# Performance work log

Hardware: AMD Instinct MI355X
Metric: run time of the kernel (lower is better)

The kernel has to match this reference:

```python
import jax, jax.numpy as jnp
import numpy as np

# cv2 GrabCut label codes
GC_BGD, GC_FGD, GC_PR_BGD, GC_PR_FGD = 0, 1, 2, 3
ITER_COUNT = 5
GAMMA = 50.0  # smoothness weight (GrabCut's standard gamma)

B, C, H, W = 2, 256, 512, 512


def setup_inputs() -> dict:
    key = jax.random.key(0)
    k1, k2 = jax.random.split(key)
    features = jax.random.normal(k1, (B, C, H, W), dtype=jnp.float32)
    mask = jax.random.randint(k2, (B, H, W), 0, 2, dtype=jnp.int32)
    return {"features": features, "mask": mask}


def _neighbor_mean(a):
    # a: (B,H,W); 4-neighbor mean with edge replication (smoothness/pairwise term)
    p = jnp.pad(a, ((0, 0), (1, 1), (1, 1)), mode="edge")
    return (p[:, :-2, 1:-1] + p[:, 2:, 1:-1] + p[:, 1:-1, :-2] + p[:, 1:-1, 2:]) * 0.25


def reference(features, mask):
    b, c, h, w = features.shape
    # take first 3 channels as pseudo-RGB image, HWC layout
    img = jnp.transpose(features[:, :3], (0, 2, 3, 1))  # (B,H,W,3)
    # cv2.normalize(..., 0, 255, NORM_MINMAX) over the whole array, then uint8 cast
    mn = img.min(axis=(1, 2, 3), keepdims=True)
    mx = img.max(axis=(1, 2, 3), keepdims=True)
    img = jnp.clip(jnp.floor((img - mn) / (mx - mn + 1e-12) * 255.0), 0.0, 255.0)

    # trimap seeding exactly as in the torch module
    tri = jnp.where(mask == 1, GC_PR_FGD, GC_PR_BGD).astype(jnp.int32)
    bh, bw = int(h * 0.1), int(w * 0.1)
    tri = tri.at[:, :bh, :].set(GC_BGD)
    tri = tri.at[:, h - bh:, :].set(GC_BGD)
    tri = tri.at[:, :, :bw].set(GC_BGD)
    tri = tri.at[:, :, w - bw:].set(GC_BGD)
    tri = tri.at[:, int(h * 0.45):int(h * 0.55), int(w * 0.45):int(w * 0.55)].set(GC_FGD)

    fixed = (tri == GC_BGD) | (tri == GC_FGD)          # hard constraints never change
    fixed_fg = (tri == GC_FGD).astype(img.dtype)
    alpha = ((tri == GC_FGD) | (tri == GC_PR_FGD)).astype(img.dtype)  # fg indicator

    # GrabCut surrogate: iteratively (1) refit fg/bg color models from current
    # labeling (GMM step collapsed to per-region mean), (2) relabel probable
    # pixels by unary (color distance) + pairwise (neighbor agreement) energy
    # -- an ICM approximation of the min-cut step.
    for _ in range(ITER_COUNT):
        a4 = alpha[..., None]                                    # (B,H,W,1)
        fg_mean = (img * a4).sum((1, 2)) / (a4.sum((1, 2)) + 1e-6)        # (B,3)
        bg_mean = (img * (1.0 - a4)).sum((1, 2)) / ((1.0 - a4).sum((1, 2)) + 1e-6)
        d_fg = ((img - fg_mean[:, None, None, :]) ** 2).sum(-1)  # (B,H,W)
        d_bg = ((img - bg_mean[:, None, None, :]) ** 2).sum(-1)
        nb = _neighbor_mean(alpha)
        score = d_bg - d_fg + GAMMA * (2.0 * nb - 1.0)           # >0 -> foreground
        new_alpha = (score > 0).astype(img.dtype)
        alpha = jnp.where(fixed, fixed_fg, new_alpha)

    return alpha  # (B,H,W) in {0,1}, float32
```

## Files before the change

kernel.cpp:

```cpp
#include <hip/hip_runtime.h>
#include <stdint.h>
#include <stddef.h>

#pragma clang fp contract(off)

#define HH 512
#define WW 512
#define HW_ 262144
#define FEAT_BSTRIDE (256*HW_)

__device__ __forceinline__ float quantf(float f, float mn, float denom) {
  float v = (f - mn) / denom * 255.0f;
  v = floorf(v);
  return fminf(fmaxf(v, 0.0f), 255.0f);
}

__device__ __forceinline__ bool is_center(int y, int x) {
  return (y >= 230) & (y < 281) & (x >= 230) & (x < 281);
}
__device__ __forceinline__ bool is_border(int y, int x) {
  return (y < 51) | (y >= 461) | (x < 51) | (x >= 461);
}

__global__ __launch_bounds__(256) void k_minmax(const float* __restrict__ feat,
                                                float2* __restrict__ mm) {
  int blk = blockIdx.x, tid = threadIdx.x;
  int b = blk >> 7, ib = blk & 127;
  const float4* base =
      reinterpret_cast<const float4*>(feat + (size_t)b * FEAT_BSTRIDE) + (size_t)ib * 1536;
  float mn = 3.4e38f, mx = -3.4e38f;
#pragma unroll
  for (int j = 0; j < 6; j++) {
    float4 v = base[tid + j * 256];
    mn = fminf(mn, fminf(fminf(v.x, v.y), fminf(v.z, v.w)));
    mx = fmaxf(mx, fmaxf(fmaxf(v.x, v.y), fmaxf(v.z, v.w)));
  }
  __shared__ float smn[256], smx[256];
  smn[tid] = mn; smx[tid] = mx;
  __syncthreads();
  for (int s = 128; s >= 1; s >>= 1) {
    if (tid < s) {
      smn[tid] = fminf(smn[tid], smn[tid + s]);
      smx[tid] = fmaxf(smx[tid], smx[tid + s]);
    }
    __syncthreads();
  }
  if (tid == 0) mm[blk] = make_float2(smn[0], smx[0]);
}

__global__ __launch_bounds__(256) void k_init(const float* __restrict__ feat,
                                              const int* __restrict__ mask,
                                              const float2* __restrict__ mm,
                                              uint32_t* __restrict__ packed,
                                              uint8_t* __restrict__ alphaA,
                                              int4* __restrict__ totals,
                                              int4* __restrict__ slot0) {
  int blk = blockIdx.x, tid = threadIdx.x;
  int b = blk >> 7;
  __shared__ float smn[128], smx[128];
  if (tid < 128) { float2 v = mm[b * 128 + tid]; smn[tid] = v.x; smx[tid] = v.y; }
  __syncthreads();
  for (int s = 64; s >= 1; s >>= 1) {
    if (tid < s) {
      smn[tid] = fminf(smn[tid], smn[tid + s]);
      smx[tid] = fmaxf(smx[tid], smx[tid + s]);
    }
    __syncthreads();
  }
  float mn = smn[0];
  float denom = (smx[0] - mn) + 1e-12f;
  const float* fb = feat + (size_t)b * FEAT_BSTRIDE;
  int a0 = 0, a1 = 0, a2 = 0, a3 = 0, t0 = 0, t1 = 0, t2 = 0;
#pragma unroll
  for (int j = 0; j < 8; j++) {
    int p = blk * 2048 + tid + j * 256;
    int pb = p & (HW_ - 1);
    int y = pb >> 9, x = pb & 511;
    int r  = (int)quantf(fb[pb], mn, denom);
    int g  = (int)quantf(fb[HW_ + pb], mn, denom);
    int bl = (int)quantf(fb[2 * HW_ + pb], mn, denom);
    packed[p] = (uint32_t)r | ((uint32_t)g << 8) | ((uint32_t)bl << 16);
    int a;
    if (is_center(y, x)) a = 1;
    else if (is_border(y, x)) a = 0;
    else a = (mask[p] == 1) ? 1 : 0;
    alphaA[p] = (uint8_t)a;
    a0 += r * a; a1 += g * a; a2 += bl * a; a3 += a;
    t0 += r; t1 += g; t2 += bl;
  }
  __shared__ int red[256][8];
  red[tid][0] = a0; red[tid][1] = a1; red[tid][2] = a2; red[tid][3] = a3;
  red[tid][4] = t0; red[tid][5] = t1; red[tid][6] = t2; red[tid][7] = 0;
  __syncthreads();
  for (int s = 128; s >= 1; s >>= 1) {
    if (tid < s) {
#pragma unroll
      for (int j = 0; j < 7; j++) red[tid][j] += red[tid + s][j];
    }
    __syncthreads();
  }
  if (tid == 0) {
    slot0[blk]  = make_int4(red[0][0], red[0][1], red[0][2], red[0][3]);
    totals[blk] = make_int4(red[0][4], red[0][5], red[0][6], 0);
  }
}

__global__ __launch_bounds__(256) void k_relabel(const uint32_t* __restrict__ packed,
                                                 const uint8_t* __restrict__ ain,
                                                 uint8_t* __restrict__ aout,
                                                 const int4* __restrict__ totals,
                                                 const int4* __restrict__ slotIn,
                                                 int4* __restrict__ slotOut,
                                                 float* __restrict__ out,
                                                 int finalIter) {
  int blk = blockIdx.x, tid = threadIdx.x;
  int b = blk >> 7;
  __shared__ int red[128][8];
  if (tid < 128) {
    int4 s = slotIn[b * 128 + tid];
    int4 t = totals[b * 128 + tid];
    red[tid][0] = s.x; red[tid][1] = s.y; red[tid][2] = s.z; red[tid][3] = s.w;
    red[tid][4] = t.x; red[tid][5] = t.y; red[tid][6] = t.z; red[tid][7] = 0;
  }
  __syncthreads();
  for (int s = 64; s >= 1; s >>= 1) {
    if (tid < s) {
#pragma unroll
      for (int j = 0; j < 7; j++) red[tid][j] += red[tid + s][j];
    }
    __syncthreads();
  }
  __shared__ float fmv[3], bmv[3];
  if (tid == 0) {
    int cnt = red[0][3];
    float fden = (float)cnt + 1e-6f;
    float bden = (float)(HW_ - cnt) + 1e-6f;
#pragma unroll
    for (int c = 0; c < 3; c++) {
      fmv[c] = (float)red[0][c] / fden;
      bmv[c] = (float)(red[0][4 + c] - red[0][c]) / bden;
    }
  }
  __syncthreads();
  float f0 = fmv[0], f1 = fmv[1], f2 = fmv[2];
  float g0 = bmv[0], g1 = bmv[1], g2 = bmv[2];
  int a0 = 0, a1 = 0, a2 = 0, a3 = 0;
#pragma unroll
  for (int j = 0; j < 8; j++) {
    int p = blk * 2048 + tid + j * 256;
    int pb = p & (HW_ - 1);
    int y = pb >> 9, x = pb & 511;
    uint32_t rgb = packed[p];
    int ri = (int)(rgb & 255u);
    int gi = (int)((rgb >> 8) & 255u);
    int bi = (int)((rgb >> 16) & 255u);
    float i0 = (float)ri, i1 = (float)gi, i2 = (float)bi;
    int up = ain[p - (y > 0 ? WW : 0)];
    int dn = ain[p + (y < HH - 1 ? WW : 0)];
    int lf = ain[p - (x > 0 ? 1 : 0)];
    int rt = ain[p + (x < WW - 1 ? 1 : 0)];
    float nb = (float)(((up + dn) + lf) + rt) * 0.25f;
    float pair = 50.0f * ((2.0f * nb) - 1.0f);
    float t0 = i0 - f0, t1 = i1 - f1, t2 = i2 - f2;
    float df = ((t0 * t0) + (t1 * t1)) + (t2 * t2);
    float u0 = i0 - g0, u1 = i1 - g1, u2 = i2 - g2;
    float db = ((u0 * u0) + (u1 * u1)) + (u2 * u2);
    float score = (db - df) + pair;
    int a;
    if (is_center(y, x)) a = 1;
    else if (is_border(y, x)) a = 0;
    else a = (score > 0.0f) ? 1 : 0;
    aout[p] = (uint8_t)a;
    if (finalIter) out[p] = (float)a;
    a0 += ri * a; a1 += gi * a; a2 += bi * a; a3 += a;
  }
  __shared__ int red2[256][4];
  red2[tid][0] = a0; red2[tid][1] = a1; red2[tid][2] = a2; red2[tid][3] = a3;
  __syncthreads();
  for (int s = 128; s >= 1; s >>= 1) {
    if (tid < s) {
#pragma unroll
      for (int j = 0; j < 4; j++) red2[tid][j] += red2[tid + s][j];
    }
    __syncthreads();
  }
  if (tid == 0) slotOut[blk] = make_int4(red2[0][0], red2[0][1], red2[0][2], red2[0][3]);
}

extern "C" void kernel_launch(void* const* d_in, const int* in_sizes, int n_in,
                              void* d_out, int out_size, void* d_ws, size_t ws_size,
                              hipStream_t stream) {
  const float* feat = (const float*)d_in[0];
  const int*   mask = (const int*)d_in[1];
  float* out = (float*)d_out;

  char* ws = (char*)d_ws;
  uint8_t*  aA     = (uint8_t*)(ws);
  uint8_t*  aB     = (uint8_t*)(ws + 524288);
  float2*   mm     = (float2*)(ws + 1048576);
  int4*     totals = (int4*)(ws + 1050624);
  int4*     slots  = (int4*)(ws + 1054720);
  uint32_t* packed = (uint32_t*)(ws + 1079296);

  k_minmax<<<256, 256, 0, stream>>>(feat, mm);
  k_init<<<256, 256, 0, stream>>>(feat, mask, mm, packed, aA, totals, slots );

  uint8_t* ain = aA;
  uint8_t* aout_buf = aB;
  for (int k = 0; k < 5; k++) {
    k_relabel<<<256, 256, 0, stream>>>(packed, ain, aout_buf, totals,
                                       slots + (size_t)k * 256,
                                       slots + (size_t)(k + 1) * 256,
                                       out, (k == 4) ? 1 : 0);
    uint8_t* tmp = ain; ain = aout_buf; aout_buf = tmp;
  }
}
```

Baseline: 611.3 us.

## Fuse all stages into one cooperative kernel with grid syncs and register-held pixels

Replaces the seven kernel launches (minmax, init, five relabels) with one cooperative kernel that uses grid-wide syncs between phases. Each thread keeps its RGB values, packed quantized colors and trimap codes in registers, so the packed buffer and the repeated mask and feature reads are gone. The min/max pass now reads only the three channel planes it needs for the assigned pixels, where the old pass read a flat float4 span. The cost is cooperative launch overhead and grid barriers, plus higher register pressure.

```diff
diff --git a/kernel.cpp b/kernel.cpp
--- a/kernel.cpp
+++ b/kernel.cpp
@@ -1,8 +1,11 @@
 #include <hip/hip_runtime.h>
+#include <hip/hip_cooperative_groups.h>
 #include <stdint.h>
 #include <stddef.h>
 
 #pragma clang fp contract(off)
+
+namespace cg = cooperative_groups;
 
 #define HH 512
 #define WW 512
@@ -22,20 +25,40 @@
   return (y < 51) | (y >= 461) | (x < 51) | (x >= 461);
 }
 
-__global__ __launch_bounds__(256) void k_minmax(const float* __restrict__ feat,
-                                                float2* __restrict__ mm) {
-  int blk = blockIdx.x, tid = threadIdx.x;
-  int b = blk >> 7, ib = blk & 127;
-  const float4* base =
-      reinterpret_cast<const float4*>(feat + (size_t)b * FEAT_BSTRIDE) + (size_t)ib * 1536;
+__global__ __launch_bounds__(256) void k_fused(
+    const float* __restrict__ feat, const int* __restrict__ mask,
+    float* __restrict__ out,
+    uint8_t* __restrict__ aA, uint8_t* __restrict__ aB,
+    float2* __restrict__ mm, int4* __restrict__ totals,
+    int4* __restrict__ slots)
+{
+  cg::grid_group grid = cg::this_grid();
+  const int blk = blockIdx.x, tid = threadIdx.x;
+  const int b = blk >> 7;
+  const float* fbp = feat + (size_t)b * FEAT_BSTRIDE;
+
+  __shared__ float smn[256], smx[256];
+  __shared__ int red[256][8];
+  __shared__ float fmv[3], bmv[3];
+
+  float fr[8], fg[8], fbl[8];
+  uint32_t code = 0;
   float mn = 3.4e38f, mx = -3.4e38f;
 #pragma unroll
-  for (int j = 0; j < 6; j++) {
-    float4 v = base[tid + j * 256];
-    mn = fminf(mn, fminf(fminf(v.x, v.y), fminf(v.z, v.w)));
-    mx = fmaxf(mx, fmaxf(fmaxf(v.x, v.y), fmaxf(v.z, v.w)));
-  }
-  __shared__ float smn[256], smx[256];
+  for (int j = 0; j < 8; j++) {
+    int p = blk * 2048 + tid + j * 256;
+    int pb = p & (HW_ - 1);
+    int y = pb >> 9, x = pb & 511;
+    float r = fbp[pb], g = fbp[HW_ + pb], bl = fbp[2 * HW_ + pb];
+    fr[j] = r; fg[j] = g; fbl[j] = bl;
+    mn = fminf(mn, fminf(r, fminf(g, bl)));
+    mx = fmaxf(mx, fmaxf(r, fmaxf(g, bl)));
+    uint32_t c2;
+    if (is_center(y, x)) c2 = 1u;
+    else if (is_border(y, x)) c2 = 2u;
+    else c2 = (mask[p] == 1) ? 3u : 0u;
+    code |= c2 << (2 * j);
+  }
   smn[tid] = mn; smx[tid] = mx;
   __syncthreads();
   for (int s = 128; s >= 1; s >>= 1) {
@@ -46,18 +69,9 @@
     __syncthreads();
   }
   if (tid == 0) mm[blk] = make_float2(smn[0], smx[0]);
-}
-
-__global__ __launch_bounds__(256) void k_init(const float* __restrict__ feat,
-                                              const int* __restrict__ mask,
-                                              const float2* __restrict__ mm,
-                                              uint32_t* __restrict__ packed,
-                                              uint8_t* __restrict__ alphaA,
-                                              int4* __restrict__ totals,
-                                              int4* __restrict__ slot0) {
-  int blk = blockIdx.x, tid = threadIdx.x;
-  int b = blk >> 7;
-  __shared__ float smn[128], smx[128];
+  __threadfence();
+  grid.sync();
+
   if (tid < 128) { float2 v = mm[b * 128 + tid]; smn[tid] = v.x; smx[tid] = v.y; }
   __syncthreads();
   for (int s = 64; s >= 1; s >>= 1) {
@@ -67,30 +81,28 @@
     }
     __syncthreads();
   }
-  float mn = smn[0];
-  float denom = (smx[0] - mn) + 1e-12f;
-  const float* fb = feat + (size_t)b * FEAT_BSTRIDE;
-  int a0 = 0, a1 = 0, a2 = 0, a3 = 0, t0 = 0, t1 = 0, t2 = 0;
-#pragma unroll
-  for (int j = 0; j < 8; j++) {
-    int p = blk * 2048 + tid + j * 256;
-    int pb = p & (HW_ - 1);
-    int y = pb >> 9, x = pb & 511;
-    int r  = (int)quantf(fb[pb], mn, denom);
-    int g  = (int)quantf(fb[HW_ + pb], mn, denom);
-    int bl = (int)quantf(fb[2 * HW_ + pb], mn, denom);
-    packed[p] = (uint32_t)r | ((uint32_t)g << 8) | ((uint32_t)bl << 16);
-    int a;
-    if (is_center(y, x)) a = 1;
-    else if (is_border(y, x)) a = 0;
-    else a = (mask[p] == 1) ? 1 : 0;
-    alphaA[p] = (uint8_t)a;
-    a0 += r * a; a1 += g * a; a2 += bl * a; a3 += a;
-    t0 += r; t1 += g; t2 += bl;
-  }
-  __shared__ int red[256][8];
-  red[tid][0] = a0; red[tid][1] = a1; red[tid][2] = a2; red[tid][3] = a3;
-  red[tid][4] = t0; red[tid][5] = t1; red[tid][6] = t2; red[tid][7] = 0;
+  float bmn = smn[0];
+  float denom = (smx[0] - bmn) + 1e-12f;
+
+  uint32_t pk[8];
+  {
+    int a0 = 0, a1 = 0, a2 = 0, a3 = 0, t0 = 0, t1 = 0, t2 = 0;
+#pragma unroll
+    for (int j = 0; j < 8; j++) {
+      int p = blk * 2048 + tid + j * 256;
+      int r  = (int)quantf(fr[j],  bmn, denom);
+      int g  = (int)quantf(fg[j],  bmn, denom);
+      int bl = (int)quantf(fbl[j], bmn, denom);
+      pk[j] = (uint32_t)r | ((uint32_t)g << 8) | ((uint32_t)bl << 16);
+      uint32_t c2 = (code >> (2 * j)) & 3u;
+      int a = (c2 == 1u || c2 == 3u) ? 1 : 0;
+      aA[p] = (uint8_t)a;
+      a0 += r * a; a1 += g * a; a2 += bl * a; a3 += a;
+      t0 += r; t1 += g; t2 += bl;
+    }
+    red[tid][0] = a0; red[tid][1] = a1; red[tid][2] = a2; red[tid][3] = a3;
+    red[tid][4] = t0; red[tid][5] = t1; red[tid][6] = t2; red[tid][7] = 0;
+  }
   __syncthreads();
   for (int s = 128; s >= 1; s >>= 1) {
     if (tid < s) {
@@ -100,91 +112,88 @@
     __syncthreads();
   }
   if (tid == 0) {
-    slot0[blk]  = make_int4(red[0][0], red[0][1], red[0][2], red[0][3]);
+    slots[blk]  = make_int4(red[0][0], red[0][1], red[0][2], red[0][3]);
     totals[blk] = make_int4(red[0][4], red[0][5], red[0][6], 0);
   }
-}
-
-__global__ __launch_bounds__(256) void k_relabel(const uint32_t* __restrict__ packed,
-                                                 const uint8_t* __restrict__ ain,
-                                                 uint8_t* __restrict__ aout,
-                                                 const int4* __restrict__ totals,
-                                                 const int4* __restrict__ slotIn,
-                                                 int4* __restrict__ slotOut,
-                                                 float* __restrict__ out,
-                                                 int finalIter) {
-  int blk = blockIdx.x, tid = threadIdx.x;
-  int b = blk >> 7;
-  __shared__ int red[128][8];
-  if (tid < 128) {
-    int4 s = slotIn[b * 128 + tid];
-    int4 t = totals[b * 128 + tid];
-    red[tid][0] = s.x; red[tid][1] = s.y; red[tid][2] = s.z; red[tid][3] = s.w;
-    red[tid][4] = t.x; red[tid][5] = t.y; red[tid][6] = t.z; red[tid][7] = 0;
-  }
-  __syncthreads();
-  for (int s = 64; s >= 1; s >>= 1) {
-    if (tid < s) {
-#pragma unroll
-      for (int j = 0; j < 7; j++) red[tid][j] += red[tid + s][j];
-    }
-    __syncthreads();
-  }
-  __shared__ float fmv[3], bmv[3];
-  if (tid == 0) {
-    int cnt = red[0][3];
-    float fden = (float)cnt + 1e-6f;
-    float bden = (float)(HW_ - cnt) + 1e-6f;
-#pragma unroll
-    for (int c = 0; c < 3; c++) {
-      fmv[c] = (float)red[0][c] / fden;
-      bmv[c] = (float)(red[0][4 + c] - red[0][c]) / bden;
-    }
-  }
-  __syncthreads();
-  float f0 = fmv[0], f1 = fmv[1], f2 = fmv[2];
-  float g0 = bmv[0], g1 = bmv[1], g2 = bmv[2];
-  int a0 = 0, a1 = 0, a2 = 0, a3 = 0;
-#pragma unroll
-  for (int j = 0; j < 8; j++) {
-    int p = blk * 2048 + tid + j * 256;
-    int pb = p & (HW_ - 1);
-    int y = pb >> 9, x = pb & 511;
-    uint32_t rgb = packed[p];
-    int ri = (int)(rgb & 255u);
-    int gi = (int)((rgb >> 8) & 255u);
-    int bi = (int)((rgb >> 16) & 255u);
-    float i0 = (float)ri, i1 = (float)gi, i2 = (float)bi;
-    int up = ain[p - (y > 0 ? WW : 0)];
-    int dn = ain[p + (y < HH - 1 ? WW : 0)];
-    int lf = ain[p - (x > 0 ? 1 : 0)];
-    int rt = ain[p + (x < WW - 1 ? 1 : 0)];
-    float nb = (float)(((up + dn) + lf) + rt) * 0.25f;
-    float pair = 50.0f * ((2.0f * nb) - 1.0f);
-    float t0 = i0 - f0, t1 = i1 - f1, t2 = i2 - f2;
-    float df = ((t0 * t0) + (t1 * t1)) + (t2 * t2);
-    float u0 = i0 - g0, u1 = i1 - g1, u2 = i2 - g2;
-    float db = ((u0 * u0) + (u1 * u1)) + (u2 * u2);
-    float score = (db - df) + pair;
-    int a;
-    if (is_center(y, x)) a = 1;
-    else if (is_border(y, x)) a = 0;
-    else a = (score > 0.0f) ? 1 : 0;
-    aout[p] = (uint8_t)a;
-    if (finalIter) out[p] = (float)a;
-    a0 += ri * a; a1 += gi * a; a2 += bi * a; a3 += a;
-  }
-  __shared__ int red2[256][4];
-  red2[tid][0] = a0; red2[tid][1] = a1; red2[tid][2] = a2; red2[tid][3] = a3;
-  __syncthreads();
-  for (int s = 128; s >= 1; s >>= 1) {
-    if (tid < s) {
-#pragma unroll
-      for (int j = 0; j < 4; j++) red2[tid][j] += red2[tid + s][j];
-    }
-    __syncthreads();
-  }
-  if (tid == 0) slotOut[blk] = make_int4(red2[0][0], red2[0][1], red2[0][2], red2[0][3]);
+  __threadfence();
+  grid.sync();
+
+  uint8_t* ain = aA;
+  uint8_t* aout = aB;
+  for (int k = 0; k < 5; k++) {
+    const int4* slotIn = slots + (size_t)k * 256;
+    int4* slotOut = slots + (size_t)(k + 1) * 256;
+    if (tid < 128) {
+      int4 s = slotIn[b * 128 + tid];
+      int4 t = totals[b * 128 + tid];
+      red[tid][0] = s.x; red[tid][1] = s.y; red[tid][2] = s.z; red[tid][3] = s.w;
+      red[tid][4] = t.x; red[tid][5] = t.y; red[tid][6] = t.z; red[tid][7] = 0;
+    }
+    __syncthreads();
+    for (int s = 64; s >= 1; s >>= 1) {
+      if (tid < s) {
+#pragma unroll
+        for (int j = 0; j < 7; j++) red[tid][j] += red[tid + s][j];
+      }
+      __syncthreads();
+    }
+    if (tid == 0) {
+      int cnt = red[0][3];
+      float fden = (float)cnt + 1e-6f;
+      float bden = (float)(HW_ - cnt) + 1e-6f;
+#pragma unroll
+      for (int c = 0; c < 3; c++) {
+        fmv[c] = (float)red[0][c] / fden;
+        bmv[c] = (float)(red[0][4 + c] - red[0][c]) / bden;
+      }
+    }
+    __syncthreads();
+    float f0 = fmv[0], f1 = fmv[1], f2 = fmv[2];
+    float g0 = bmv[0], g1 = bmv[1], g2 = bmv[2];
+    int a0 = 0, a1 = 0, a2 = 0, a3 = 0;
+#pragma unroll
+    for (int j = 0; j < 8; j++) {
+      int p = blk * 2048 + tid + j * 256;
+      int pb = p & (HW_ - 1);
+      int y = pb >> 9, x = pb & 511;
+      uint32_t rgb = pk[j];
+      int ri = (int)(rgb & 255u);
+      int gi = (int)((rgb >> 8) & 255u);
+      int bi = (int)((rgb >> 16) & 255u);
+      float i0 = (float)ri, i1 = (float)gi, i2 = (float)bi;
+      int up = ain[p - (y > 0 ? WW : 0)];
+      int dn = ain[p + (y < HH - 1 ? WW : 0)];
+      int lf = ain[p - (x > 0 ? 1 : 0)];
+      int rt = ain[p + (x < WW - 1 ? 1 : 0)];
+      float nb = (float)(((up + dn) + lf) + rt) * 0.25f;
+      float pair = 50.0f * ((2.0f * nb) - 1.0f);
+      float t0 = i0 - f0, t1 = i1 - f1, t2 = i2 - f2;
+      float df = ((t0 * t0) + (t1 * t1)) + (t2 * t2);
+      float u0 = i0 - g0, u1 = i1 - g1, u2 = i2 - g2;
+      float db = ((u0 * u0) + (u1 * u1)) + (u2 * u2);
+      float score = (db - df) + pair;
+      uint32_t c2 = (code >> (2 * j)) & 3u;
+      int a;
+      if (c2 == 1u) a = 1;
+      else if (c2 == 2u) a = 0;
+      else a = (score > 0.0f) ? 1 : 0;
+      aout[p] = (uint8_t)a;
+      if (k == 4) out[p] = (float)a;
+      a0 += ri * a; a1 += gi * a; a2 += bi * a; a3 += a;
+    }
+    red[tid][0] = a0; red[tid][1] = a1; red[tid][2] = a2; red[tid][3] = a3;
+    __syncthreads();
+    for (int s = 128; s >= 1; s >>= 1) {
+      if (tid < s) {
+#pragma unroll
+        for (int j = 0; j < 4; j++) red[tid][j] += red[tid + s][j];
+      }
+      __syncthreads();
+    }
+    if (tid == 0) slotOut[blk] = make_int4(red[0][0], red[0][1], red[0][2], red[0][3]);
+    if (k < 4) { __threadfence(); grid.sync(); }
+    uint8_t* t = ain; ain = aout; aout = t;
+  }
 }
 
 extern "C" void kernel_launch(void* const* d_in, const int* in_sizes, int n_in,
@@ -195,23 +204,14 @@
   float* out = (float*)d_out;
 
   char* ws = (char*)d_ws;
-  uint8_t*  aA     = (uint8_t*)(ws);
-  uint8_t*  aB     = (uint8_t*)(ws + 524288);
-  float2*   mm     = (float2*)(ws + 1048576);
-  int4*     totals = (int4*)(ws + 1050624);
-  int4*     slots  = (int4*)(ws + 1054720);
-  uint32_t* packed = (uint32_t*)(ws + 1079296);
-
-  k_minmax<<<256, 256, 0, stream>>>(feat, mm);
-  k_init<<<256, 256, 0, stream>>>(feat, mask, mm, packed, aA, totals, slots );
-
-  uint8_t* ain = aA;
-  uint8_t* aout_buf = aB;
-  for (int k = 0; k < 5; k++) {
-    k_relabel<<<256, 256, 0, stream>>>(packed, ain, aout_buf, totals,
-                                       slots + (size_t)k * 256,
-                                       slots + (size_t)(k + 1) * 256,
-                                       out, (k == 4) ? 1 : 0);
-    uint8_t* tmp = ain; ain = aout_buf; aout_buf = tmp;
-  }
-}
+  uint8_t* aA     = (uint8_t*)(ws);
+  uint8_t* aB     = (uint8_t*)(ws + 524288);
+  float2*  mm     = (float2*)(ws + 1048576);
+  int4*    totals = (int4*)(ws + 1050624);
+  int4*    slots  = (int4*)(ws + 1054720);
+
+  void* args[] = {(void*)&feat, (void*)&mask, (void*)&out, (void*)&aA, (void*)&aB,
+                  (void*)&mm, (void*)&totals, (void*)&slots};
+  hipLaunchCooperativeKernel((const void*)k_fused, dim3(256), dim3(256),
+                             args, 0, stream);
+}
```

After: 875.7 us. 1.43x slower.

## Vectorize init/relabel, stage alpha rows in LDS, use wave-shuffle reductions

Applied to the files above, without the earlier changes.

Init and relabel now process four contiguous pixels per thread with float4/uint4/uint32 vector loads and stores, and launch 512 blocks instead of 256. Relabel stages the up, center and down alpha rows for its two output rows into shared memory, so neighbor lookups become packed-byte extracts instead of scattered byte loads. The shared-memory tree reductions are replaced by wavefront shuffle sums plus a small cross-wave combine, which cuts barrier count. The slot and packed workspace offsets are moved to fit the doubled number of per-block partials.

```diff
diff --git a/kernel.cpp b/kernel.cpp
--- a/kernel.cpp
+++ b/kernel.cpp
@@ -20,6 +20,12 @@
 }
 __device__ __forceinline__ bool is_border(int y, int x) {
   return (y < 51) | (y >= 461) | (x < 51) | (x >= 461);
+}
+
+__device__ __forceinline__ int wsum(int v) {
+#pragma unroll
+  for (int m = 32; m >= 1; m >>= 1) v += __shfl_xor(v, m);
+  return v;
 }
 
 __global__ __launch_bounds__(256) void k_minmax(const float* __restrict__ feat,
@@ -56,7 +62,7 @@
                                               int4* __restrict__ totals,
                                               int4* __restrict__ slot0) {
   int blk = blockIdx.x, tid = threadIdx.x;
-  int b = blk >> 7;
+  int b = blk >> 8;
   __shared__ float smn[128], smx[128];
   if (tid < 128) { float2 v = mm[b * 128 + tid]; smn[tid] = v.x; smx[tid] = v.y; }
   __syncthreads();
@@ -69,39 +75,58 @@
   }
   float mn = smn[0];
   float denom = (smx[0] - mn) + 1e-12f;
-  const float* fb = feat + (size_t)b * FEAT_BSTRIDE;
+
+  int pix = blk * 1024 + tid * 4;
+  int pb = pix & (HW_ - 1);
+  int y = pb >> 9, xb = pb & 511;
+  const float* fbp = feat + (size_t)b * FEAT_BSTRIDE;
+  float4 cr = *reinterpret_cast<const float4*>(fbp + pb);
+  float4 cg = *reinterpret_cast<const float4*>(fbp + HW_ + pb);
+  float4 cb = *reinterpret_cast<const float4*>(fbp + 2 * HW_ + pb);
+  int4 mk = *reinterpret_cast<const int4*>(mask + pix);
+  float rs[4] = {cr.x, cr.y, cr.z, cr.w};
+  float gs[4] = {cg.x, cg.y, cg.z, cg.w};
+  float bs[4] = {cb.x, cb.y, cb.z, cb.w};
+  int mks[4] = {mk.x, mk.y, mk.z, mk.w};
   int a0 = 0, a1 = 0, a2 = 0, a3 = 0, t0 = 0, t1 = 0, t2 = 0;
-#pragma unroll
-  for (int j = 0; j < 8; j++) {
-    int p = blk * 2048 + tid + j * 256;
-    int pb = p & (HW_ - 1);
-    int y = pb >> 9, x = pb & 511;
-    int r  = (int)quantf(fb[pb], mn, denom);
-    int g  = (int)quantf(fb[HW_ + pb], mn, denom);
-    int bl = (int)quantf(fb[2 * HW_ + pb], mn, denom);
-    packed[p] = (uint32_t)r | ((uint32_t)g << 8) | ((uint32_t)bl << 16);
+  uint32_t pkw[4];
+  uint32_t aw = 0;
+#pragma unroll
+  for (int i = 0; i < 4; i++) {
+    int r  = (int)quantf(rs[i], mn, denom);
+    int g  = (int)quantf(gs[i], mn, denom);
+    int bl = (int)quantf(bs[i], mn, denom);
+    pkw[i] = (uint32_t)r | ((uint32_t)g << 8) | ((uint32_t)bl << 16);
+    int x = xb + i;
     int a;
     if (is_center(y, x)) a = 1;
     else if (is_border(y, x)) a = 0;
-    else a = (mask[p] == 1) ? 1 : 0;
-    alphaA[p] = (uint8_t)a;
+    else a = (mks[i] == 1) ? 1 : 0;
+    aw |= (uint32_t)a << (8 * i);
     a0 += r * a; a1 += g * a; a2 += bl * a; a3 += a;
     t0 += r; t1 += g; t2 += bl;
   }
-  __shared__ int red[256][8];
-  red[tid][0] = a0; red[tid][1] = a1; red[tid][2] = a2; red[tid][3] = a3;
-  red[tid][4] = t0; red[tid][5] = t1; red[tid][6] = t2; red[tid][7] = 0;
-  __syncthreads();
-  for (int s = 128; s >= 1; s >>= 1) {
-    if (tid < s) {
-#pragma unroll
-      for (int j = 0; j < 7; j++) red[tid][j] += red[tid + s][j];
+  *reinterpret_cast<uint4*>(packed + pix) = make_uint4(pkw[0], pkw[1], pkw[2], pkw[3]);
+  *reinterpret_cast<uint32_t*>(alphaA + pix) = aw;
+
+  a0 = wsum(a0); a1 = wsum(a1); a2 = wsum(a2); a3 = wsum(a3);
+  t0 = wsum(t0); t1 = wsum(t1); t2 = wsum(t2);
+  __shared__ int xw[4][8];
+  int wid = tid >> 6, lane = tid & 63;
+  if (lane == 0) {
+    xw[wid][0] = a0; xw[wid][1] = a1; xw[wid][2] = a2; xw[wid][3] = a3;
+    xw[wid][4] = t0; xw[wid][5] = t1; xw[wid][6] = t2;
+  }
+  __syncthreads();
+  if (tid == 0) {
+    int s0 = 0, s1 = 0, s2 = 0, s3 = 0, u0 = 0, u1 = 0, u2 = 0;
+#pragma unroll
+    for (int w = 0; w < 4; w++) {
+      s0 += xw[w][0]; s1 += xw[w][1]; s2 += xw[w][2]; s3 += xw[w][3];
+      u0 += xw[w][4]; u1 += xw[w][5]; u2 += xw[w][6];
     }
-    __syncthreads();
-  }
-  if (tid == 0) {
-    slot0[blk]  = make_int4(red[0][0], red[0][1], red[0][2], red[0][3]);
-    totals[blk] = make_int4(red[0][4], red[0][5], red[0][6], 0);
+    slot0[blk]  = make_int4(s0, s1, s2, s3);
+    totals[blk] = make_int4(u0, u1, u2, 0);
   }
 }
 
@@ -114,51 +139,74 @@
                                                  float* __restrict__ out,
                                                  int finalIter) {
   int blk = blockIdx.x, tid = threadIdx.x;
-  int b = blk >> 7;
-  __shared__ int red[128][8];
-  if (tid < 128) {
-    int4 s = slotIn[b * 128 + tid];
-    int4 t = totals[b * 128 + tid];
-    red[tid][0] = s.x; red[tid][1] = s.y; red[tid][2] = s.z; red[tid][3] = s.w;
-    red[tid][4] = t.x; red[tid][5] = t.y; red[tid][6] = t.z; red[tid][7] = 0;
-  }
-  __syncthreads();
-  for (int s = 64; s >= 1; s >>= 1) {
-    if (tid < s) {
-#pragma unroll
-      for (int j = 0; j < 7; j++) red[tid][j] += red[tid + s][j];
-    }
-    __syncthreads();
-  }
-  __shared__ float fmv[3], bmv[3];
-  if (tid == 0) {
-    int cnt = red[0][3];
-    float fden = (float)cnt + 1e-6f;
-    float bden = (float)(HW_ - cnt) + 1e-6f;
-#pragma unroll
-    for (int c = 0; c < 3; c++) {
-      fmv[c] = (float)red[0][c] / fden;
-      bmv[c] = (float)(red[0][4 + c] - red[0][c]) / bden;
-    }
-  }
-  __syncthreads();
-  float f0 = fmv[0], f1 = fmv[1], f2 = fmv[2];
-  float g0 = bmv[0], g1 = bmv[1], g2 = bmv[2];
+  int b = blk >> 8;
+  int r0 = (blk & 255) * 2;
+
+  __shared__ uint32_t arowW[4 * 128];
+  {
+    int row_i = tid >> 6;
+    int src_row = r0 - 1 + row_i;
+    src_row = src_row < 0 ? 0 : (src_row > 511 ? 511 : src_row);
+    reinterpret_cast<uint2*>(arowW)[tid] = *reinterpret_cast<const uint2*>(
+        ain + (size_t)b * HW_ + src_row * 512 + (tid & 63) * 8);
+  }
+
+  int4 sv = slotIn[b * 256 + tid];
+  int4 tv = totals[b * 256 + tid];
+  int v0 = wsum(sv.x), v1 = wsum(sv.y), v2 = wsum(sv.z), v3 = wsum(sv.w);
+  int v4 = wsum(tv.x), v5 = wsum(tv.y), v6 = wsum(tv.z);
+  __shared__ int xw[4][8];
+  int wid = tid >> 6, lane = tid & 63;
+  if (lane == 0) {
+    xw[wid][0] = v0; xw[wid][1] = v1; xw[wid][2] = v2; xw[wid][3] = v3;
+    xw[wid][4] = v4; xw[wid][5] = v5; xw[wid][6] = v6;
+  }
+  __syncthreads();
+  int s0 = xw[0][0] + xw[1][0] + xw[2][0] + xw[3][0];
+  int s1 = xw[0][1] + xw[1][1] + xw[2][1] + xw[3][1];
+  int s2 = xw[0][2] + xw[1][2] + xw[2][2] + xw[3][2];
+  int s3 = xw[0][3] + xw[1][3] + xw[2][3] + xw[3][3];
+  int s4 = xw[0][4] + xw[1][4] + xw[2][4] + xw[3][4];
+  int s5 = xw[0][5] + xw[1][5] + xw[2][5] + xw[3][5];
+  int s6 = xw[0][6] + xw[1][6] + xw[2][6] + xw[3][6];
+  int cnt = s3;
+  float fden = (float)cnt + 1e-6f;
+  float bden = (float)(HW_ - cnt) + 1e-6f;
+  float f0 = (float)s0 / fden;
+  float f1 = (float)s1 / fden;
+  float f2 = (float)s2 / fden;
+  float g0 = (float)(s4 - s0) / bden;
+  float g1 = (float)(s5 - s1) / bden;
+  float g2 = (float)(s6 - s2) / bden;
+
+  int lr = tid >> 7;
+  int q  = tid & 127;
+  int x0 = q * 4;
+  int yy = r0 + lr;
+  uint32_t uw = arowW[lr * 128 + q];
+  uint32_t cw = arowW[(lr + 1) * 128 + q];
+  uint32_t dw = arowW[(lr + 2) * 128 + q];
+  const uint8_t* arowB = reinterpret_cast<const uint8_t*>(arowW);
+  int lfb = arowB[(lr + 1) * 512 + (x0 > 0 ? x0 - 1 : 0)];
+  int rtb = arowB[(lr + 1) * 512 + (x0 + 4 < 512 ? x0 + 4 : 511)];
+
+  int pix = b * HW_ + yy * 512 + x0;
+  uint4 pk4 = *reinterpret_cast<const uint4*>(packed + pix);
+  uint32_t pka[4] = {pk4.x, pk4.y, pk4.z, pk4.w};
   int a0 = 0, a1 = 0, a2 = 0, a3 = 0;
-#pragma unroll
-  for (int j = 0; j < 8; j++) {
-    int p = blk * 2048 + tid + j * 256;
-    int pb = p & (HW_ - 1);
-    int y = pb >> 9, x = pb & 511;
-    uint32_t rgb = packed[p];
+  uint32_t awout = 0;
+  float fouts[4];
+#pragma unroll
+  for (int i = 0; i < 4; i++) {
+    uint32_t rgb = pka[i];
     int ri = (int)(rgb & 255u);
     int gi = (int)((rgb >> 8) & 255u);
     int bi = (int)((rgb >> 16) & 255u);
     float i0 = (float)ri, i1 = (float)gi, i2 = (float)bi;
-    int up = ain[p - (y > 0 ? WW : 0)];
-    int dn = ain[p + (y < HH - 1 ? WW : 0)];
-    int lf = ain[p - (x > 0 ? 1 : 0)];
-    int rt = ain[p + (x < WW - 1 ? 1 : 0)];
+    int up = (int)((uw >> (8 * i)) & 255u);
+    int dn = (int)((dw >> (8 * i)) & 255u);
+    int lf = (i == 0) ? lfb : (int)((cw >> (8 * (i - 1))) & 255u);
+    int rt = (i == 3) ? rtb : (int)((cw >> (8 * (i + 1))) & 255u);
     float nb = (float)(((up + dn) + lf) + rt) * 0.25f;
     float pair = 50.0f * ((2.0f * nb) - 1.0f);
     float t0 = i0 - f0, t1 = i1 - f1, t2 = i2 - f2;
@@ -166,25 +214,30 @@
     float u0 = i0 - g0, u1 = i1 - g1, u2 = i2 - g2;
     float db = ((u0 * u0) + (u1 * u1)) + (u2 * u2);
     float score = (db - df) + pair;
+    int x = x0 + i;
     int a;
-    if (is_center(y, x)) a = 1;
-    else if (is_border(y, x)) a = 0;
+    if (is_center(yy, x)) a = 1;
+    else if (is_border(yy, x)) a = 0;
     else a = (score > 0.0f) ? 1 : 0;
-    aout[p] = (uint8_t)a;
-    if (finalIter) out[p] = (float)a;
+    awout |= (uint32_t)a << (8 * i);
+    fouts[i] = (float)a;
     a0 += ri * a; a1 += gi * a; a2 += bi * a; a3 += a;
   }
-  __shared__ int red2[256][4];
-  red2[tid][0] = a0; red2[tid][1] = a1; red2[tid][2] = a2; red2[tid][3] = a3;
-  __syncthreads();
-  for (int s = 128; s >= 1; s >>= 1) {
-    if (tid < s) {
-#pragma unroll
-      for (int j = 0; j < 4; j++) red2[tid][j] += red2[tid + s][j];
-    }
-    __syncthreads();
-  }
-  if (tid == 0) slotOut[blk] = make_int4(red2[0][0], red2[0][1], red2[0][2], red2[0][3]);
+  *reinterpret_cast<uint32_t*>(aout + pix) = awout;
+  if (finalIter)
+    *reinterpret_cast<float4*>(out + pix) = make_float4(fouts[0], fouts[1], fouts[2], fouts[3]);
+
+  a0 = wsum(a0); a1 = wsum(a1); a2 = wsum(a2); a3 = wsum(a3);
+  __syncthreads();
+  if (lane == 0) { xw[wid][0] = a0; xw[wid][1] = a1; xw[wid][2] = a2; xw[wid][3] = a3; }
+  __syncthreads();
+  if (tid == 0) {
+    int o0 = xw[0][0] + xw[1][0] + xw[2][0] + xw[3][0];
+    int o1 = xw[0][1] + xw[1][1] + xw[2][1] + xw[3][1];
+    int o2 = xw[0][2] + xw[1][2] + xw[2][2] + xw[3][2];
+    int o3 = xw[0][3] + xw[1][3] + xw[2][3] + xw[3][3];
+    slotOut[blk] = make_int4(o0, o1, o2, o3);
+  }
 }
 
 extern "C" void kernel_launch(void* const* d_in, const int* in_sizes, int n_in,
@@ -199,18 +252,18 @@
   uint8_t*  aB     = (uint8_t*)(ws + 524288);
   float2*   mm     = (float2*)(ws + 1048576);
   int4*     totals = (int4*)(ws + 1050624);
-  int4*     slots  = (int4*)(ws + 1054720);
-  uint32_t* packed = (uint32_t*)(ws + 1079296);
+  int4*     slots  = (int4*)(ws + 1058816);
+  uint32_t* packed = (uint32_t*)(ws + 1107968);
 
   k_minmax<<<256, 256, 0, stream>>>(feat, mm);
-  k_init<<<256, 256, 0, stream>>>(feat, mask, mm, packed, aA, totals, slots );
+  k_init<<<512, 256, 0, stream>>>(feat, mask, mm, packed, aA, totals, slots );
 
   uint8_t* ain = aA;
   uint8_t* aout_buf = aB;
   for (int k = 0; k < 5; k++) {
-    k_relabel<<<256, 256, 0, stream>>>(packed, ain, aout_buf, totals,
-                                       slots + (size_t)k * 256,
-                                       slots + (size_t)(k + 1) * 256,
+    k_relabel<<<512, 256, 0, stream>>>(packed, ain, aout_buf, totals,
+                                       slots + (size_t)k * 512,
+                                       slots + (size_t)(k + 1) * 512,
                                        out, (k == 4) ? 1 : 0);
     uint8_t* tmp = ain; ain = aout_buf; aout_buf = tmp;
   }
```

After: 590.5 us. 1.04x faster.
